# Kernel tuning notes

Measured on AMD Instinct MI355X. Metric: run time of the kernel, lower is better.

The kernel has to match this reference:

```python
import math
import jax, jax.numpy as jnp
import numpy as np

B, S, D, H, DFF = 2, 2048, 2048, 16, 8192
DH = D // H
EPS = 1e-5


def setup_inputs() -> dict:
    key = jax.random.key(0)
    ks = jax.random.split(key, 12)
    std = 0.02
    inp = {
        "x": jax.random.normal(ks[0], (B, S, D), dtype=jnp.float32),
        # causal mask: 1 = allowed, 0 = masked
        "attn_mask": jnp.tril(jnp.ones((S, S), dtype=jnp.int32))[None, None],
        "ln1_g": jnp.ones((D,), jnp.float32),
        "ln1_b": jnp.zeros((D,), jnp.float32),
        "wq": jax.random.normal(ks[1], (D, D), jnp.float32) * std,
        "bq": jnp.zeros((D,), jnp.float32),
        "wk": jax.random.normal(ks[2], (D, D), jnp.float32) * std,
        "bk": jnp.zeros((D,), jnp.float32),
        "wv": jax.random.normal(ks[3], (D, D), jnp.float32) * std,
        "bv": jnp.zeros((D,), jnp.float32),
        "wo": jax.random.normal(ks[4], (D, D), jnp.float32) * std,
        "bo": jnp.zeros((D,), jnp.float32),
        "ln2_g": jnp.ones((D,), jnp.float32),
        "ln2_b": jnp.zeros((D,), jnp.float32),
        "w_in": jax.random.normal(ks[5], (D, DFF), jnp.float32) * std,
        "b_in": jnp.zeros((DFF,), jnp.float32),
        "w_out": jax.random.normal(ks[6], (DFF, D), jnp.float32) * std,
        "b_out": jnp.zeros((D,), jnp.float32),
    }
    return inp


def _layernorm(x, g, b):
    m = jnp.mean(x, axis=-1, keepdims=True)
    v = jnp.mean(jnp.square(x - m), axis=-1, keepdims=True)
    return (x - m) * jax.lax.rsqrt(v + EPS) * g + b


def _block(x, attn_mask, ln1_g, ln1_b, wq, bq, wk, bk, wv, bv, wo, bo,
           ln2_g, ln2_b, w_in, b_in, w_out, b_out):
    b_, s_, d_ = x.shape
    # --- attention sublayer (pre-norm) ---
    xn = _layernorm(x, ln1_g, ln1_b)
    q = (xn @ wq + bq).reshape(b_, s_, H, DH)
    k = (xn @ wk + bk).reshape(b_, s_, H, DH)
    v = (xn @ wv + bv).reshape(b_, s_, H, DH)
    scores = jnp.einsum("bqhd,bkhd->bhqk", q, k) / math.sqrt(DH)  # [B,H,S,S]
    scores = jnp.where(attn_mask == 0, -jnp.inf, scores)
    probs = jax.nn.softmax(scores, axis=-1)
    attn = jnp.einsum("bhqk,bkhd->bqhd", probs, v).reshape(b_, s_, d_)
    x = x + (attn @ wo + bo)
    # --- MLP sublayer (pre-norm) ---
    xn = _layernorm(x, ln2_g, ln2_b)
    h = jax.nn.gelu(xn @ w_in + b_in, approximate=False)
    x = x + (h @ w_out + b_out)
    return x


def reference(x, attn_mask, ln1_g, ln1_b, wq, bq, wk, bk, wv, bv, wo, bo,
              ln2_g, ln2_b, w_in, b_in, w_out, b_out):
    return _block(x, attn_mask, ln1_g, ln1_b, wq, bq, wk, bk, wv, bv, wo, bo,
                  ln2_g, ln2_b, w_in, b_in, w_out, b_out)
```

## Files before the change

### kernel.cpp

```cpp
#include <hip/hip_runtime.h>
#include <hip/hip_bf16.h>

#define BB   2
#define SS   2048
#define DD   2048
#define HH   16
#define DHH  128
#define DFF  8192
#define MM   (BB*SS)

typedef __hip_bfloat16 bf16;
typedef __bf16 bf16x8 __attribute__((ext_vector_type(8)));
typedef float  f32x4 __attribute__((ext_vector_type(4)));

__device__ __forceinline__ void gl2lds16(const void* g, void* lds_uniform_base) {
    __builtin_amdgcn_global_load_lds(
        (const __attribute__((address_space(1))) void*)g,
        (__attribute__((address_space(3))) void*)lds_uniform_base,
        16, 0, 0);
}

__global__ __launch_bounds__(256) void ln_kernel(const float* __restrict__ x,
                                                 const float* __restrict__ g,
                                                 const float* __restrict__ b,
                                                 bf16* __restrict__ out) {
    int row = blockIdx.x, tid = threadIdx.x;
    const float4* xr = (const float4*)(x + (size_t)row * DD);
    float4 v0 = xr[tid];
    float4 v1 = xr[tid + 256];
    float s  = v0.x + v0.y + v0.z + v0.w + v1.x + v1.y + v1.z + v1.w;
    float s2 = v0.x*v0.x + v0.y*v0.y + v0.z*v0.z + v0.w*v0.w
             + v1.x*v1.x + v1.y*v1.y + v1.z*v1.z + v1.w*v1.w;
    #pragma unroll
    for (int m = 32; m >= 1; m >>= 1) { s += __shfl_xor(s, m); s2 += __shfl_xor(s2, m); }
    __shared__ float red[8];
    int wv = tid >> 6;
    if ((tid & 63) == 0) { red[wv] = s; red[wv + 4] = s2; }
    __syncthreads();
    s  = red[0] + red[1] + red[2] + red[3];
    s2 = red[4] + red[5] + red[6] + red[7];
    float mean = s * (1.0f / DD);
    float rs = rsqrtf(s2 * (1.0f / DD) - mean * mean + 1e-5f);
    bf16* o = out + (size_t)row * DD;
    int c0 = tid * 4, c1 = (tid + 256) * 4;
    float a0[4] = {v0.x, v0.y, v0.z, v0.w};
    float a1[4] = {v1.x, v1.y, v1.z, v1.w};
    #pragma unroll
    for (int j = 0; j < 4; j++) {
        o[c0 + j] = __float2bfloat16((a0[j] - mean) * rs * g[c0 + j] + b[c0 + j]);
        o[c1 + j] = __float2bfloat16((a1[j] - mean) * rs * g[c1 + j] + b[c1 + j]);
    }
}

__global__ __launch_bounds__(256) void transpose_cast(const float* __restrict__ W,
                                                      bf16* __restrict__ Wt,
                                                      int K, int N) {
    __shared__ float t[32][33];
    int n0 = blockIdx.x * 32, k0 = blockIdx.y * 32;
    int tx = threadIdx.x, ty = threadIdx.y;
    #pragma unroll
    for (int i = 0; i < 4; i++)
        t[ty + i * 8][tx] = W[(size_t)(k0 + ty + i * 8) * N + n0 + tx];
    __syncthreads();
    #pragma unroll
    for (int i = 0; i < 4; i++)
        Wt[(size_t)(n0 + ty + i * 8) * K + k0 + tx] = __float2bfloat16(t[tx][ty + i * 8]);
}

__global__ __launch_bounds__(256) void transpose_v(const bf16* __restrict__ v,
                                                   bf16* __restrict__ vt) {
    __shared__ bf16 t[32][33];
    int s0 = blockIdx.x * 32, d0 = blockIdx.y * 32;
    int bh = blockIdx.z;
    int b = bh >> 4, h = bh & 15;
    int tx = threadIdx.x, ty = threadIdx.y;
    #pragma unroll
    for (int i = 0; i < 4; i++)
        t[ty + i * 8][tx] = v[(size_t)(b * SS + s0 + ty + i * 8) * DD + h * DHH + d0 + tx];
    __syncthreads();
    #pragma unroll
    for (int i = 0; i < 4; i++)
        vt[(size_t)((b * HH + h) * DHH + d0 + ty + i * 8) * SS + s0 + tx] = t[tx][ty + i * 8];
}

__global__ __launch_bounds__(256) void gemm_bt(const bf16* __restrict__ A,
                                               const bf16* __restrict__ Bt,
                                               const float* __restrict__ bias,
                                               const float* __restrict__ resid,
                                               void* __restrict__ Cout,
                                               int M, int N, int K, int epi) {
    __shared__ __align__(16) bf16 As[128 * 32];
    __shared__ __align__(16) bf16 Bs[128 * 32];
    int tid = threadIdx.x;
    int lane = tid & 63, wave = tid >> 6;
    int quad = lane >> 4, l15 = lane & 15;
    int wm = wave >> 1, wn = wave & 1;
    int bm0 = blockIdx.y * 128, bn0 = blockIdx.x * 128;
    const bf16* Ag = A + (size_t)bm0 * K;
    const bf16* Bg = Bt + (size_t)bn0 * K;
    f32x4 acc[4][4] = {};

    for (int kt = 0; kt < K; kt += 32) {
        __syncthreads();
        #pragma unroll
        for (int i = 0; i < 2; i++) {
            int chunk = i * 256 + tid;
            int row = chunk >> 2, c8 = chunk & 3;
            gl2lds16(Ag + (size_t)row * K + kt + c8 * 8, As + (i * 256 + wave * 64) * 8);
        }
        #pragma unroll
        for (int i = 0; i < 2; i++) {
            int chunk = i * 256 + tid;
            int row = chunk >> 2, c8 = chunk & 3;
            gl2lds16(Bg + (size_t)row * K + kt + c8 * 8, Bs + (i * 256 + wave * 64) * 8);
        }
        __syncthreads();
        bf16x8 af[4], bfr[4];
        #pragma unroll
        for (int mt = 0; mt < 4; mt++)
            af[mt] = *(const bf16x8*)(const void*)&As[(wm * 64 + mt * 16 + l15) * 32 + quad * 8];
        #pragma unroll
        for (int nt = 0; nt < 4; nt++)
            bfr[nt] = *(const bf16x8*)(const void*)&Bs[(wn * 64 + nt * 16 + l15) * 32 + quad * 8];
        #pragma unroll
        for (int mt = 0; mt < 4; mt++)
            #pragma unroll
            for (int nt = 0; nt < 4; nt++)
                acc[mt][nt] = __builtin_amdgcn_mfma_f32_16x16x32_bf16(af[mt], bfr[nt], acc[mt][nt], 0, 0, 0);
    }

    #pragma unroll
    for (int nt = 0; nt < 4; nt++) {
        int col = bn0 + wn * 64 + nt * 16 + l15;
        float bv = bias[col];
        #pragma unroll
        for (int mt = 0; mt < 4; mt++) {
            #pragma unroll
            for (int r = 0; r < 4; r++) {
                int row = bm0 + wm * 64 + mt * 16 + quad * 4 + r;
                size_t idx = (size_t)row * N + col;
                float v = acc[mt][nt][r] + bv;
                if (epi == 0) {
                    ((bf16*)Cout)[idx] = __float2bfloat16(v);
                } else if (epi == 1) {
                    ((float*)Cout)[idx] = v + resid[idx];
                } else {
                    float gv = 0.5f * v * (1.0f + erff(v * 0.70710678118654752f));
                    ((bf16*)Cout)[idx] = __float2bfloat16(gv);
                }
            }
        }
    }
}

__global__ __launch_bounds__(512) void flash_attn(const bf16* __restrict__ qb,
                                                  const bf16* __restrict__ kb,
                                                  const bf16* __restrict__ vt,
                                                  bf16* __restrict__ out) {
    __shared__ __align__(16) bf16 Qs[128 * 128];
    __shared__ __align__(16) bf16 Ks[128 * 128];
    __shared__ __align__(16) bf16 Vs[128 * 128];
    __shared__ __align__(16) bf16 Ps[8 * 16 * 128];
    int tid = threadIdx.x;
    int lane = tid & 63, wave = tid >> 6;
    int quad = lane >> 4, l15 = lane & 15;
    int xr = blockIdx.x;
    int t = (xr & 1) ? (15 - (xr >> 1)) : (xr >> 1);
    int q0 = t * 128;
    int h = blockIdx.y, b = blockIdx.z;
    int jlast = t;
    const float scale = 0.088388347648318447f;

    int srow = tid >> 4;
    int sgrp = (tid & 15) ^ (srow & 15);

    #pragma unroll
    for (int i = 0; i < 4; i++) {
        int row = i * 32 + srow;
        gl2lds16(qb + (size_t)(b * SS + q0 + row) * DD + h * DHH + sgrp * 8,
                 Qs + i * 4096 + wave * 512);
    }

    f32x4 oacc[8] = {};
    float mrun[4] = {-1e30f, -1e30f, -1e30f, -1e30f};
    float lrun[4] = {0.f, 0.f, 0.f, 0.f};

    for (int j = 0; j <= jlast; j++) {
        __syncthreads();
        #pragma unroll
        for (int i = 0; i < 4; i++) {
            int row = i * 32 + srow;
            gl2lds16(kb + (size_t)(b * SS + j * 128 + row) * DD + h * DHH + sgrp * 8,
                     Ks + i * 4096 + wave * 512);
        }
        #pragma unroll
        for (int i = 0; i < 4; i++) {
            int row = i * 32 + srow;
            gl2lds16(vt + (size_t)((b * HH + h) * DHH + row) * SS + j * 128 + sgrp * 8,
                     Vs + i * 4096 + wave * 512);
        }
        __syncthreads();

        f32x4 sacc[8] = {};
        bf16x8 aq[4];
        #pragma unroll
        for (int kc = 0; kc < 4; kc++)
            aq[kc] = *(const bf16x8*)(const void*)&Qs[(wave * 16 + l15) * 128 + (((kc * 4 + quad) ^ l15) * 8)];
        #pragma unroll
        for (int n = 0; n < 8; n++)
            #pragma unroll
            for (int kc = 0; kc < 4; kc++) {
                bf16x8 bk = *(const bf16x8*)(const void*)&Ks[(n * 16 + l15) * 128 + (((kc * 4 + quad) ^ l15) * 8)];
                sacc[n] = __builtin_amdgcn_mfma_f32_16x16x32_bf16(aq[kc], bk, sacc[n], 0, 0, 0);
            }

        float mx[4] = {-1e30f, -1e30f, -1e30f, -1e30f};
        #pragma unroll
        for (int n = 0; n < 8; n++)
            #pragma unroll
            for (int r = 0; r < 4; r++) {
                float v = sacc[n][r] * scale;
                if (j == jlast) {
                    int kl = n * 16 + l15;
                    int ql = wave * 16 + quad * 4 + r;
                    if (kl > ql) v = -1e30f;
                }
                sacc[n][r] = v;
                mx[r] = fmaxf(mx[r], v);
            }
        #pragma unroll
        for (int r = 0; r < 4; r++) {
            mx[r] = fmaxf(mx[r], __shfl_xor(mx[r], 1));
            mx[r] = fmaxf(mx[r], __shfl_xor(mx[r], 2));
            mx[r] = fmaxf(mx[r], __shfl_xor(mx[r], 4));
            mx[r] = fmaxf(mx[r], __shfl_xor(mx[r], 8));
        }
        float alpha[4], rsum[4];
        #pragma unroll
        for (int r = 0; r < 4; r++) {
            float mn = fmaxf(mrun[r], mx[r]);
            alpha[r] = __expf(mrun[r] - mn);
            mrun[r] = mn;
            rsum[r] = 0.f;
        }
        #pragma unroll
        for (int n = 0; n < 8; n++)
            #pragma unroll
            for (int r = 0; r < 4; r++) {
                float p = __expf(sacc[n][r] - mrun[r]);
                sacc[n][r] = p;
                rsum[r] += p;
            }
        #pragma unroll
        for (int r = 0; r < 4; r++) {
            rsum[r] += __shfl_xor(rsum[r], 1);
            rsum[r] += __shfl_xor(rsum[r], 2);
            rsum[r] += __shfl_xor(rsum[r], 4);
            rsum[r] += __shfl_xor(rsum[r], 8);
            lrun[r] = lrun[r] * alpha[r] + rsum[r];
        }
        #pragma unroll
        for (int n = 0; n < 8; n++)
            #pragma unroll
            for (int r = 0; r < 4; r++)
                oacc[n][r] *= alpha[r];

        #pragma unroll
        for (int n = 0; n < 8; n++)
            #pragma unroll
            for (int r = 0; r < 4; r++) {
                int rowp = quad * 4 + r;
                int g = 2 * n + (l15 >> 3);
                Ps[wave * 2048 + rowp * 128 + ((g ^ rowp) * 8) + (l15 & 7)] =
                    __float2bfloat16(sacc[n][r]);
            }
        asm volatile("s_waitcnt lgkmcnt(0)" ::: "memory");

        bf16x8 ap[4];
        #pragma unroll
        for (int kc = 0; kc < 4; kc++)
            ap[kc] = *(const bf16x8*)(const void*)&Ps[wave * 2048 + l15 * 128 + (((kc * 4 + quad) ^ l15) * 8)];
        #pragma unroll
        for (int n = 0; n < 8; n++)
            #pragma unroll
            for (int kc = 0; kc < 4; kc++) {
                bf16x8 bv = *(const bf16x8*)(const void*)&Vs[(n * 16 + l15) * 128 + (((kc * 4 + quad) ^ l15) * 8)];
                oacc[n] = __builtin_amdgcn_mfma_f32_16x16x32_bf16(ap[kc], bv, oacc[n], 0, 0, 0);
            }
    }

    #pragma unroll
    for (int n = 0; n < 8; n++)
        #pragma unroll
        for (int r = 0; r < 4; r++) {
            float v = oacc[n][r] / lrun[r];
            out[(size_t)(b * SS + q0 + wave * 16 + quad * 4 + r) * DD + h * DHH + n * 16 + l15] =
                __float2bfloat16(v);
        }
}

extern "C" void kernel_launch(void* const* d_in, const int* in_sizes, int n_in,
                              void* d_out, int out_size, void* d_ws, size_t ws_size,
                              hipStream_t stream) {
    (void)in_sizes; (void)n_in; (void)out_size; (void)ws_size;
    const float* x     = (const float*)d_in[0];
    const float* ln1_g = (const float*)d_in[2];
    const float* ln1_b = (const float*)d_in[3];
    const float* wq    = (const float*)d_in[4];
    const float* bq    = (const float*)d_in[5];
    const float* wk    = (const float*)d_in[6];
    const float* bk    = (const float*)d_in[7];
    const float* wv    = (const float*)d_in[8];
    const float* bv    = (const float*)d_in[9];
    const float* wo    = (const float*)d_in[10];
    const float* bo    = (const float*)d_in[11];
    const float* ln2_g = (const float*)d_in[12];
    const float* ln2_b = (const float*)d_in[13];
    const float* w_in  = (const float*)d_in[14];
    const float* b_in  = (const float*)d_in[15];
    const float* w_out = (const float*)d_in[16];
    const float* b_out = (const float*)d_in[17];
    float* out = (float*)d_out;

    char* ws = (char*)d_ws;
    const size_t MB = 1024 * 1024;
    bf16*  wt   = (bf16*)(ws + 0 * MB);
    bf16*  xn   = (bf16*)(ws + 32 * MB);
    bf16*  qb   = (bf16*)(ws + 48 * MB);
    float* x1   = (float*)(ws + 64 * MB);
    bf16*  kbuf = (bf16*)(ws + 96 * MB);
    bf16*  vbuf = (bf16*)(ws + 112 * MB);
    bf16*  vtb  = (bf16*)(ws + 128 * MB);
    bf16*  hb   = (bf16*)(ws + 96 * MB);
    bf16*  att  = xn;
    bf16*  xn2  = qb;

    dim3 t256(256), t32x8(32, 8);

    ln_kernel<<<MM, t256, 0, stream>>>(x, ln1_g, ln1_b, xn);

    transpose_cast<<<dim3(DD / 32, DD / 32), t32x8, 0, stream>>>(wq, wt, DD, DD);
    gemm_bt<<<dim3(DD / 128, MM / 128), t256, 0, stream>>>(xn, wt, bq, nullptr, qb, MM, DD, DD, 0);
    transpose_cast<<<dim3(DD / 32, DD / 32), t32x8, 0, stream>>>(wk, wt, DD, DD);
    gemm_bt<<<dim3(DD / 128, MM / 128), t256, 0, stream>>>(xn, wt, bk, nullptr, kbuf, MM, DD, DD, 0);
    transpose_cast<<<dim3(DD / 32, DD / 32), t32x8, 0, stream>>>(wv, wt, DD, DD);
    gemm_bt<<<dim3(DD / 128, MM / 128), t256, 0, stream>>>(xn, wt, bv, nullptr, vbuf, MM, DD, DD, 0);
    transpose_v<<<dim3(SS / 32, DHH / 32, BB * HH), t32x8, 0, stream>>>(vbuf, vtb);

    flash_attn<<<dim3(SS / 128, HH, BB), dim3(512), 0, stream>>>(qb, kbuf, vtb, att);

    transpose_cast<<<dim3(DD / 32, DD / 32), t32x8, 0, stream>>>(wo, wt, DD, DD);
    gemm_bt<<<dim3(DD / 128, MM / 128), t256, 0, stream>>>(att, wt, bo, x, x1, MM, DD, DD, 1);

    ln_kernel<<<MM, t256, 0, stream>>>(x1, ln2_g, ln2_b, xn2);

    transpose_cast<<<dim3(DFF / 32, DD / 32), t32x8, 0, stream>>>(w_in, wt, DD, DFF);
    gemm_bt<<<dim3(DFF / 128, MM / 128), t256, 0, stream>>>(xn2, wt, b_in, nullptr, hb, MM, DFF, DD, 2);

    transpose_cast<<<dim3(DD / 32, DFF / 32), t32x8, 0, stream>>>(w_out, wt, DFF, DD);
    gemm_bt<<<dim3(DD / 128, MM / 128), t256, 0, stream>>>(hb, wt, b_out, x1, out, MM, DD, DFF, 1);
}
```

Before: 1.089 ms.

## Fuse Q/K/V projections into one GEMM and stage bf16 epilogue through LDS

The three separate Q, K and V projection GEMMs are merged into a single GEMM with N=6144. The transposed weights are laid out contiguously and the biases are concatenated, and flash attention and the V transpose now read from the packed QKV buffer with a row stride of 6144. The bf16 epilogues (plain and GELU) now stage accumulators through a padded LDS tile, so each lane writes 16 contiguous bf16 values as two 128-bit stores instead of scattered 2-byte stores. This trades extra LDS use and an extra small kernel for fewer launches, better wave fill in the QKV GEMM, and coalesced output writes. The workspace layout is rearranged to fit the larger QKV buffer.

```diff
diff --git a/kernel.cpp b/kernel.cpp
--- a/kernel.cpp
+++ b/kernel.cpp
@@ -8,6 +8,7 @@
 #define DHH  128
 #define DFF  8192
 #define MM   (BB*SS)
+#define QKD  6144
 
 typedef __hip_bfloat16 bf16;
 typedef __bf16 bf16x8 __attribute__((ext_vector_type(8)));
@@ -67,7 +68,15 @@
         Wt[(size_t)(n0 + ty + i * 8) * K + k0 + tx] = __float2bfloat16(t[tx][ty + i * 8]);
 }
 
-__global__ __launch_bounds__(256) void transpose_v(const bf16* __restrict__ v,
+__global__ __launch_bounds__(256) void concat3(const float* __restrict__ a,
+                                               const float* __restrict__ b,
+                                               const float* __restrict__ c,
+                                               float* __restrict__ o) {
+    int i = blockIdx.x * 256 + threadIdx.x;
+    o[i] = i < 2048 ? a[i] : (i < 4096 ? b[i - 2048] : c[i - 4096]);
+}
+
+__global__ __launch_bounds__(256) void transpose_v(const bf16* __restrict__ qkv,
                                                    bf16* __restrict__ vt) {
     __shared__ bf16 t[32][33];
     int s0 = blockIdx.x * 32, d0 = blockIdx.y * 32;
@@ -76,7 +85,7 @@
     int tx = threadIdx.x, ty = threadIdx.y;
     #pragma unroll
     for (int i = 0; i < 4; i++)
-        t[ty + i * 8][tx] = v[(size_t)(b * SS + s0 + ty + i * 8) * DD + h * DHH + d0 + tx];
+        t[ty + i * 8][tx] = qkv[(size_t)(b * SS + s0 + ty + i * 8) * QKD + 4096 + h * DHH + d0 + tx];
     __syncthreads();
     #pragma unroll
     for (int i = 0; i < 4; i++)
@@ -91,6 +100,7 @@
                                                int M, int N, int K, int epi) {
     __shared__ __align__(16) bf16 As[128 * 32];
     __shared__ __align__(16) bf16 Bs[128 * 32];
+    __shared__ __align__(16) float Es[4 * 16 * 68];
     int tid = threadIdx.x;
     int lane = tid & 63, wave = tid >> 6;
     int quad = lane >> 4, l15 = lane & 15;
@@ -129,32 +139,58 @@
                 acc[mt][nt] = __builtin_amdgcn_mfma_f32_16x16x32_bf16(af[mt], bfr[nt], acc[mt][nt], 0, 0, 0);
     }
 
-    #pragma unroll
-    for (int nt = 0; nt < 4; nt++) {
-        int col = bn0 + wn * 64 + nt * 16 + l15;
-        float bv = bias[col];
+    if (epi == 1) {
+        #pragma unroll
+        for (int nt = 0; nt < 4; nt++) {
+            int col = bn0 + wn * 64 + nt * 16 + l15;
+            float bv = bias[col];
+            #pragma unroll
+            for (int mt = 0; mt < 4; mt++)
+                #pragma unroll
+                for (int r = 0; r < 4; r++) {
+                    int row = bm0 + wm * 64 + mt * 16 + quad * 4 + r;
+                    size_t idx = (size_t)row * N + col;
+                    ((float*)Cout)[idx] = acc[mt][nt][r] + bv + resid[idx];
+                }
+        }
+    } else {
+        float bv[4];
+        #pragma unroll
+        for (int nt = 0; nt < 4; nt++) bv[nt] = bias[bn0 + wn * 64 + nt * 16 + l15];
+        int rr = lane >> 2, cc = lane & 3;
         #pragma unroll
         for (int mt = 0; mt < 4; mt++) {
             #pragma unroll
-            for (int r = 0; r < 4; r++) {
-                int row = bm0 + wm * 64 + mt * 16 + quad * 4 + r;
-                size_t idx = (size_t)row * N + col;
-                float v = acc[mt][nt][r] + bv;
-                if (epi == 0) {
-                    ((bf16*)Cout)[idx] = __float2bfloat16(v);
-                } else if (epi == 1) {
-                    ((float*)Cout)[idx] = v + resid[idx];
-                } else {
-                    float gv = 0.5f * v * (1.0f + erff(v * 0.70710678118654752f));
-                    ((bf16*)Cout)[idx] = __float2bfloat16(gv);
-                }
-            }
+            for (int nt = 0; nt < 4; nt++)
+                #pragma unroll
+                for (int r = 0; r < 4; r++)
+                    Es[wave * 1088 + (quad * 4 + r) * 68 + nt * 16 + l15] = acc[mt][nt][r] + bv[nt];
+            asm volatile("s_waitcnt lgkmcnt(0)" ::: "memory");
+            float vals[16];
+            #pragma unroll
+            for (int j4 = 0; j4 < 4; j4++) {
+                float4 f = *(const float4*)&Es[wave * 1088 + rr * 68 + cc * 16 + j4 * 4];
+                vals[j4 * 4 + 0] = f.x; vals[j4 * 4 + 1] = f.y;
+                vals[j4 * 4 + 2] = f.z; vals[j4 * 4 + 3] = f.w;
+            }
+            asm volatile("s_waitcnt lgkmcnt(0)" ::: "memory");
+            union { bf16 h[16]; uint4 u[2]; } ob;
+            #pragma unroll
+            for (int j = 0; j < 16; j++) {
+                float v = vals[j];
+                if (epi == 2) v = 0.5f * v * (1.0f + erff(v * 0.70710678118654752f));
+                ob.h[j] = __float2bfloat16(v);
+            }
+            int grow = bm0 + wm * 64 + mt * 16 + rr;
+            int gcol = bn0 + wn * 64 + cc * 16;
+            uint4* dst = (uint4*)((bf16*)Cout + (size_t)grow * N + gcol);
+            dst[0] = ob.u[0];
+            dst[1] = ob.u[1];
         }
     }
 }
 
-__global__ __launch_bounds__(512) void flash_attn(const bf16* __restrict__ qb,
-                                                  const bf16* __restrict__ kb,
+__global__ __launch_bounds__(512) void flash_attn(const bf16* __restrict__ qkv,
                                                   const bf16* __restrict__ vt,
                                                   bf16* __restrict__ out) {
     __shared__ __align__(16) bf16 Qs[128 * 128];
@@ -174,10 +210,13 @@
     int srow = tid >> 4;
     int sgrp = (tid & 15) ^ (srow & 15);
 
+    const bf16* qb = qkv + h * DHH;
+    const bf16* kb = qkv + 2048 + h * DHH;
+
     #pragma unroll
     for (int i = 0; i < 4; i++) {
         int row = i * 32 + srow;
-        gl2lds16(qb + (size_t)(b * SS + q0 + row) * DD + h * DHH + sgrp * 8,
+        gl2lds16(qb + (size_t)(b * SS + q0 + row) * QKD + sgrp * 8,
                  Qs + i * 4096 + wave * 512);
     }
 
@@ -190,7 +229,7 @@
         #pragma unroll
         for (int i = 0; i < 4; i++) {
             int row = i * 32 + srow;
-            gl2lds16(kb + (size_t)(b * SS + j * 128 + row) * DD + h * DHH + sgrp * 8,
+            gl2lds16(kb + (size_t)(b * SS + j * 128 + row) * QKD + sgrp * 8,
                      Ks + i * 4096 + wave * 512);
         }
         #pragma unroll
@@ -326,28 +365,27 @@
     const size_t MB = 1024 * 1024;
     bf16*  wt   = (bf16*)(ws + 0 * MB);
     bf16*  xn   = (bf16*)(ws + 32 * MB);
-    bf16*  qb   = (bf16*)(ws + 48 * MB);
-    float* x1   = (float*)(ws + 64 * MB);
-    bf16*  kbuf = (bf16*)(ws + 96 * MB);
-    bf16*  vbuf = (bf16*)(ws + 112 * MB);
-    bf16*  vtb  = (bf16*)(ws + 128 * MB);
-    bf16*  hb   = (bf16*)(ws + 96 * MB);
+    bf16*  qkvb = (bf16*)(ws + 48 * MB);
+    bf16*  vtb  = (bf16*)(ws + 96 * MB);
+    float* x1   = (float*)(ws + 112 * MB);
+    float* bcat = (float*)(ws + 144 * MB);
+    bf16*  hb   = (bf16*)(ws + 48 * MB);
     bf16*  att  = xn;
-    bf16*  xn2  = qb;
+    bf16*  xn2  = xn;
 
     dim3 t256(256), t32x8(32, 8);
 
     ln_kernel<<<MM, t256, 0, stream>>>(x, ln1_g, ln1_b, xn);
 
     transpose_cast<<<dim3(DD / 32, DD / 32), t32x8, 0, stream>>>(wq, wt, DD, DD);
-    gemm_bt<<<dim3(DD / 128, MM / 128), t256, 0, stream>>>(xn, wt, bq, nullptr, qb, MM, DD, DD, 0);
-    transpose_cast<<<dim3(DD / 32, DD / 32), t32x8, 0, stream>>>(wk, wt, DD, DD);
-    gemm_bt<<<dim3(DD / 128, MM / 128), t256, 0, stream>>>(xn, wt, bk, nullptr, kbuf, MM, DD, DD, 0);
-    transpose_cast<<<dim3(DD / 32, DD / 32), t32x8, 0, stream>>>(wv, wt, DD, DD);
-    gemm_bt<<<dim3(DD / 128, MM / 128), t256, 0, stream>>>(xn, wt, bv, nullptr, vbuf, MM, DD, DD, 0);
-    transpose_v<<<dim3(SS / 32, DHH / 32, BB * HH), t32x8, 0, stream>>>(vbuf, vtb);
-
-    flash_attn<<<dim3(SS / 128, HH, BB), dim3(512), 0, stream>>>(qb, kbuf, vtb, att);
+    transpose_cast<<<dim3(DD / 32, DD / 32), t32x8, 0, stream>>>(wk, wt + 2048 * 2048, DD, DD);
+    transpose_cast<<<dim3(DD / 32, DD / 32), t32x8, 0, stream>>>(wv, wt + 2 * 2048 * 2048, DD, DD);
+    concat3<<<QKD / 256, t256, 0, stream>>>(bq, bk, bv, bcat);
+    gemm_bt<<<dim3(QKD / 128, MM / 128), t256, 0, stream>>>(xn, wt, bcat, nullptr, qkvb, MM, QKD, DD, 0);
+
+    transpose_v<<<dim3(SS / 32, DHH / 32, BB * HH), t32x8, 0, stream>>>(qkvb, vtb);
+
+    flash_attn<<<dim3(SS / 128, HH, BB), dim3(512), 0, stream>>>(qkvb, vtb, att);
 
     transpose_cast<<<dim3(DD / 32, DD / 32), t32x8, 0, stream>>>(wo, wt, DD, DD);
     gemm_bt<<<dim3(DD / 128, MM / 128), t256, 0, stream>>>(att, wt, bo, x, x1, MM, DD, DD, 1);
```

Result: no change. 1.075 ms (-1.3%).
